# Kernel optimization log

Measured on AMD Instinct MI355X. Metric: run time of the kernel, lower is better.

Reference implementation:

```python
import jax, jax.numpy as jnp
import numpy as np

S = 32.0
M = 0.35
T = 0.2
EPS = 1e-12  # F.normalize default eps


def _l2_normalize(x, axis):
    n = jnp.sqrt(jnp.sum(x * x, axis=axis, keepdims=True))
    return x / jnp.maximum(n, EPS)


def setup_inputs() -> dict:
    key = jax.random.key(0)
    k1, k2, k3 = jax.random.split(key, 3)
    B, D, C = 512, 512, 100000
    return {
        "input": jax.random.normal(k1, (B, D), dtype=jnp.float32),
        "weight": jax.random.normal(k2, (C, D), dtype=jnp.float32),
        "label": jax.random.randint(k3, (B,), 0, C, dtype=jnp.int64),
    }


def reference(input, weight, label):
    B = input.shape[0]
    # normalized GEMM -> cosine similarities [B, C]
    cos_theta = _l2_normalize(input, 1) @ _l2_normalize(weight, 1).T
    cos_theta = jnp.clip(cos_theta, -1.0, 1.0)
    rows = jnp.arange(B)
    gt = cos_theta[rows, label][:, None]  # [B, 1]
    # MV-AM: boost hard (mis-classified-ish) logits: cos > gt - m
    hard = cos_theta > (gt - M)
    cos_theta = jnp.where(hard, (T + 1.0) * cos_theta + T, cos_theta)
    # easy_margin=False -> final_gt = gt - m; scatter into label column
    final_gt = gt - M
    cos_theta = cos_theta.at[rows, label].set(final_gt[:, 0])
    return cos_theta * S
```

## Files before the change

kernel.cpp:

```cpp
#include <hip/hip_runtime.h>
#include <hip/hip_bf16.h>


#define S_SCALE 32.0f
#define MARGIN  0.35f
#define T_BOOST 0.2f
#define EPSN    1e-12f

constexpr int Bn = 512;
constexpr int Dn = 512;
constexpr int Cn = 100000;

constexpr int BM = 256, BN = 128, BK = 32;
constexpr int PAD = 40;

typedef __attribute__((ext_vector_type(8))) short bf16x8;
typedef __attribute__((ext_vector_type(4))) float f32x4;

static __device__ inline unsigned short f32_bf16(float f) {
    unsigned int u = __float_as_uint(f);
    u += 0x7FFFu + ((u >> 16) & 1u);
    return (unsigned short)(u >> 16);
}

__global__ __launch_bounds__(256) void prep_kernel(const float* __restrict__ in,
                                                   const float* __restrict__ w,
                                                   const int* __restrict__ label,
                                                   float* __restrict__ gt,
                                                   unsigned short* __restrict__ in_h) {
    int b = blockIdx.x;
    int t = threadIdx.x;
    const float* irow = in + (size_t)b * Dn;
    int lab = label[b];
    const float* wrow = w + (size_t)lab * Dn;
    float x0 = irow[t], x1 = irow[t + 256];
    float y0 = wrow[t], y1 = wrow[t + 256];
    float s_ii = x0 * x0 + x1 * x1;
    float s_ww = y0 * y0 + y1 * y1;
    float s_iw = x0 * y0 + x1 * y1;
    #pragma unroll
    for (int off = 32; off; off >>= 1) {
        s_ii += __shfl_xor(s_ii, off);
        s_ww += __shfl_xor(s_ww, off);
        s_iw += __shfl_xor(s_iw, off);
    }
    __shared__ float r0[4], r1[4], r2[4], bc[1];
    int wid = t >> 6;
    if ((t & 63) == 0) { r0[wid] = s_ii; r1[wid] = s_ww; r2[wid] = s_iw; }
    __syncthreads();
    if (t == 0) {
        float a = r0[0] + r0[1] + r0[2] + r0[3];
        float c = r1[0] + r1[1] + r1[2] + r1[3];
        float d = r2[0] + r2[1] + r2[2] + r2[3];
        float inv_i = 1.0f / fmaxf(sqrtf(a), EPSN);
        float g = d * inv_i / fmaxf(sqrtf(c), EPSN);
        g = fminf(fmaxf(g, -1.0f), 1.0f);
        gt[b] = g;
        bc[0] = inv_i;
    }
    __syncthreads();
    float inv_i = bc[0];
    in_h[(size_t)b * Dn + t]       = f32_bf16(x0 * inv_i);
    in_h[(size_t)b * Dn + t + 256] = f32_bf16(x1 * inv_i);
}

__global__ __launch_bounds__(256) void winv_kernel(const float* __restrict__ w,
                                                   float* __restrict__ winv) {
    int row  = blockIdx.x * 4 + (threadIdx.x >> 6);
    int lane = threadIdx.x & 63;
    const float* wr = w + (size_t)row * Dn;
    f32x4 v0 = *(const f32x4*)(wr + lane * 4);
    f32x4 v1 = *(const f32x4*)(wr + 256 + lane * 4);
    float s = 0.f;
    #pragma unroll
    for (int i = 0; i < 4; ++i) s += v0[i] * v0[i] + v1[i] * v1[i];
    #pragma unroll
    for (int off = 32; off; off >>= 1) s += __shfl_xor(s, off);
    if (lane == 0) winv[row] = 1.0f / fmaxf(sqrtf(s), EPSN);
}

__global__ __launch_bounds__(512) void gemm_kernel(const unsigned short* __restrict__ in_h,
                                                   const float* __restrict__ w,
                                                   const float* __restrict__ winv,
                                                   const float* __restrict__ gt,
                                                   const int* __restrict__ label,
                                                   float* __restrict__ out) {
    __shared__ unsigned short As[BM * PAD];
    __shared__ unsigned short Bs[BN * PAD];

    int bm = blockIdx.x;
    int bn = blockIdx.y;
    int t = threadIdx.x;
    int wid = t >> 6, lane = t & 63;
    int wm = wid >> 1, wn = wid & 1;
    int l15 = lane & 15, lk = lane >> 4;

    f32x4 acc[4][4] = {};

    int arow = t >> 2, akg = t & 3;
    int brow = t >> 2, bkg = t & 3;
    int bc_glob = bn * BN + brow;
    if (bc_glob >= Cn) bc_glob = Cn - 1;
    const float* bsrc_row = w + (size_t)bc_glob * Dn;
    float bscale = winv[bc_glob];

    for (int kt = 0; kt < Dn; kt += BK) {
        {
            bf16x8 v = *(const bf16x8*)(in_h + ((size_t)(bm * BM + arow) * Dn + kt + akg * 8));
            *(bf16x8*)&As[arow * PAD + akg * 8] = v;
            int row2 = arow + 128;
            bf16x8 v2 = *(const bf16x8*)(in_h + ((size_t)(bm * BM + row2) * Dn + kt + akg * 8));
            *(bf16x8*)&As[row2 * PAD + akg * 8] = v2;
        }
        {
            const float* src = bsrc_row + kt + bkg * 8;
            f32x4 f0 = *(const f32x4*)src;
            f32x4 f1 = *(const f32x4*)(src + 4);
            bf16x8 hv;
            #pragma unroll
            for (int i = 0; i < 4; ++i) {
                hv[i]     = (short)f32_bf16(f0[i] * bscale);
                hv[4 + i] = (short)f32_bf16(f1[i] * bscale);
            }
            *(bf16x8*)&Bs[brow * PAD + bkg * 8] = hv;
        }
        __syncthreads();
        bf16x8 a[4], bb[4];
        #pragma unroll
        for (int mf = 0; mf < 4; ++mf)
            a[mf] = *(const bf16x8*)&As[(wm * 64 + mf * 16 + l15) * PAD + lk * 8];
        #pragma unroll
        for (int nf = 0; nf < 4; ++nf)
            bb[nf] = *(const bf16x8*)&Bs[(wn * 64 + nf * 16 + l15) * PAD + lk * 8];
        #pragma unroll
        for (int mf = 0; mf < 4; ++mf)
            #pragma unroll
            for (int nf = 0; nf < 4; ++nf)
                acc[mf][nf] = __builtin_amdgcn_mfma_f32_16x16x32_bf16(a[mf], bb[nf], acc[mf][nf], 0, 0, 0);
        __syncthreads();
    }

    #pragma unroll
    for (int mf = 0; mf < 4; ++mf) {
        int brow_base = bm * BM + wm * 64 + mf * 16 + lk * 4;
        #pragma unroll
        for (int r = 0; r < 4; ++r) {
            int b_row = brow_base + r;
            float g   = gt[b_row];
            int lab   = label[b_row];
            float thr = g - MARGIN;
            float gv  = thr * S_SCALE;
            size_t obase = (size_t)b_row * Cn;
            #pragma unroll
            for (int nf = 0; nf < 4; ++nf) {
                int c = bn * BN + wn * 64 + nf * 16 + l15;
                if (c < Cn) {
                    float cosv = acc[mf][nf][r];
                    cosv = fminf(fmaxf(cosv, -1.0f), 1.0f);
                    float o;
                    if (c == lab)          o = gv;
                    else if (cosv > thr)   o = ((T_BOOST + 1.0f) * cosv + T_BOOST) * S_SCALE;
                    else                   o = cosv * S_SCALE;
                    out[obase + c] = o;
                }
            }
        }
    }
}

extern "C" void kernel_launch(void* const* d_in, const int* in_sizes, int n_in,
                              void* d_out, int out_size, void* d_ws, size_t ws_size,
                              hipStream_t stream) {
    const float* in  = (const float*)d_in[0];
    const float* w   = (const float*)d_in[1];
    const int* label = (const int*)d_in[2];
    float* out = (float*)d_out;

    char* ws = (char*)d_ws;
    float* gt   = (float*)ws;
    float* winv = (float*)(ws + 4096);
    unsigned short* in_h = (unsigned short*)(ws + 4096 + 400384);

    prep_kernel<<<dim3(Bn), dim3(256), 0, stream>>>(in, w, label, gt, in_h);
    winv_kernel<<<dim3(Cn / 4), dim3(256), 0, stream>>>(w, winv);
    dim3 grid(2, (Cn + BN - 1) / BN);
    gemm_kernel<<<grid, dim3(512), 0, stream>>>(in_h, w, winv, gt, label, out);
}
```

Measured before the change: 187.1 us.

## Fuse weight-norm into GEMM with full-K swizzled LDS tile, drop winv kernel

Removes the separate winv kernel. Each GEMM block now loads its 64 weight rows for the full K=512 once, computes their norms in-register, and stores normalized bf16 into an XOR-swizzled LDS tile. The block covers all 512 batch rows, so weights are read once instead of twice, and the K loop has no per-step syncs. A operands are read directly from global (L2-resident in_h) rather than staged in LDS. This trades a large 64KB LDS tile and more accumulator registers for fewer global weight passes and one fewer launch.

```diff
diff --git a/kernel.cpp b/kernel.cpp
--- a/kernel.cpp
+++ b/kernel.cpp
@@ -10,9 +10,7 @@
 constexpr int Bn = 512;
 constexpr int Dn = 512;
 constexpr int Cn = 100000;
-
-constexpr int BM = 256, BN = 128, BK = 32;
-constexpr int PAD = 40;
+constexpr int BN = 64;
 
 typedef __attribute__((ext_vector_type(8))) short bf16x8;
 typedef __attribute__((ext_vector_type(4))) float f32x4;
@@ -64,103 +62,96 @@
     in_h[(size_t)b * Dn + t + 256] = f32_bf16(x1 * inv_i);
 }
 
-__global__ __launch_bounds__(256) void winv_kernel(const float* __restrict__ w,
-                                                   float* __restrict__ winv) {
-    int row  = blockIdx.x * 4 + (threadIdx.x >> 6);
-    int lane = threadIdx.x & 63;
-    const float* wr = w + (size_t)row * Dn;
-    f32x4 v0 = *(const f32x4*)(wr + lane * 4);
-    f32x4 v1 = *(const f32x4*)(wr + 256 + lane * 4);
-    float s = 0.f;
-    #pragma unroll
-    for (int i = 0; i < 4; ++i) s += v0[i] * v0[i] + v1[i] * v1[i];
-    #pragma unroll
-    for (int off = 32; off; off >>= 1) s += __shfl_xor(s, off);
-    if (lane == 0) winv[row] = 1.0f / fmaxf(sqrtf(s), EPSN);
-}
+__global__ __launch_bounds__(512, 4) void gemm_kernel(const unsigned short* __restrict__ in_h,
+                                                      const float* __restrict__ w,
+                                                      const float* __restrict__ gt,
+                                                      const int* __restrict__ label,
+                                                      float* __restrict__ out) {
+    __shared__ unsigned short Bs[BN * 512];
+    char* bsb = (char*)Bs;
+    int t = threadIdx.x, wid = t >> 6, lane = t & 63;
+    int cbase = blockIdx.x * BN;
 
-__global__ __launch_bounds__(512) void gemm_kernel(const unsigned short* __restrict__ in_h,
-                                                   const float* __restrict__ w,
-                                                   const float* __restrict__ winv,
-                                                   const float* __restrict__ gt,
-                                                   const int* __restrict__ label,
-                                                   float* __restrict__ out) {
-    __shared__ unsigned short As[BM * PAD];
-    __shared__ unsigned short Bs[BN * PAD];
+    {
+        int rl = (wid << 3) | (lane >> 3);
+        int rg = cbase + rl; if (rg >= Cn) rg = Cn - 1;
+        const float* wr = w + (size_t)rg * Dn;
+        int kc = lane & 7;
+        f32x4 vd[16];
+        #pragma unroll
+        for (int i = 0; i < 8; ++i) {
+            vd[2*i]   = *(const f32x4*)(wr + kc * 8 + i * 64);
+            vd[2*i+1] = *(const f32x4*)(wr + kc * 8 + i * 64 + 4);
+        }
+        float s = 0.f;
+        #pragma unroll
+        for (int j = 0; j < 16; ++j)
+            s += vd[j][0]*vd[j][0] + vd[j][1]*vd[j][1] + vd[j][2]*vd[j][2] + vd[j][3]*vd[j][3];
+        s += __shfl_xor(s, 1); s += __shfl_xor(s, 2); s += __shfl_xor(s, 4);
+        float invn = 1.0f / fmaxf(sqrtf(s), EPSN);
+        #pragma unroll
+        for (int i = 0; i < 8; ++i) {
+            bf16x8 hv;
+            #pragma unroll
+            for (int j = 0; j < 4; ++j) {
+                hv[j]     = (short)f32_bf16(vd[2*i][j]   * invn);
+                hv[4 + j] = (short)f32_bf16(vd[2*i+1][j] * invn);
+            }
+            int off = ((rl << 10) + (kc << 4) + (i << 7)) ^ ((rl & 7) << 4);
+            *(bf16x8*)(bsb + off) = hv;
+        }
+    }
+    __syncthreads();
 
-    int bm = blockIdx.x;
-    int bn = blockIdx.y;
-    int t = threadIdx.x;
-    int wid = t >> 6, lane = t & 63;
     int wm = wid >> 1, wn = wid & 1;
     int l15 = lane & 15, lk = lane >> 4;
+    const unsigned short* abase = in_h + (size_t)(wm * 128 + l15) * Dn + lk * 8;
+    int brow0 = wn * 32 + l15;
 
-    f32x4 acc[4][4] = {};
+    f32x4 acc[8][2];
+    #pragma unroll
+    for (int m = 0; m < 8; ++m)
+        #pragma unroll
+        for (int n = 0; n < 2; ++n) acc[m][n] = (f32x4){0.f, 0.f, 0.f, 0.f};
 
-    int arow = t >> 2, akg = t & 3;
-    int brow = t >> 2, bkg = t & 3;
-    int bc_glob = bn * BN + brow;
-    if (bc_glob >= Cn) bc_glob = Cn - 1;
-    const float* bsrc_row = w + (size_t)bc_glob * Dn;
-    float bscale = winv[bc_glob];
-
-    for (int kt = 0; kt < Dn; kt += BK) {
-        {
-            bf16x8 v = *(const bf16x8*)(in_h + ((size_t)(bm * BM + arow) * Dn + kt + akg * 8));
-            *(bf16x8*)&As[arow * PAD + akg * 8] = v;
-            int row2 = arow + 128;
-            bf16x8 v2 = *(const bf16x8*)(in_h + ((size_t)(bm * BM + row2) * Dn + kt + akg * 8));
-            *(bf16x8*)&As[row2 * PAD + akg * 8] = v2;
+    #pragma unroll
+    for (int kt = 0; kt < Dn; kt += 32) {
+        bf16x8 a[8], b[2];
+        #pragma unroll
+        for (int mf = 0; mf < 8; ++mf)
+            a[mf] = *(const bf16x8*)(abase + mf * 16 * Dn + kt);
+        #pragma unroll
+        for (int nf = 0; nf < 2; ++nf) {
+            int br = brow0 + nf * 16;
+            int off = ((br << 10) + kt * 2 + (lk << 4)) ^ ((br & 7) << 4);
+            b[nf] = *(const bf16x8*)(bsb + off);
         }
-        {
-            const float* src = bsrc_row + kt + bkg * 8;
-            f32x4 f0 = *(const f32x4*)src;
-            f32x4 f1 = *(const f32x4*)(src + 4);
-            bf16x8 hv;
+        #pragma unroll
+        for (int mf = 0; mf < 8; ++mf)
             #pragma unroll
-            for (int i = 0; i < 4; ++i) {
-                hv[i]     = (short)f32_bf16(f0[i] * bscale);
-                hv[4 + i] = (short)f32_bf16(f1[i] * bscale);
-            }
-            *(bf16x8*)&Bs[brow * PAD + bkg * 8] = hv;
-        }
-        __syncthreads();
-        bf16x8 a[4], bb[4];
-        #pragma unroll
-        for (int mf = 0; mf < 4; ++mf)
-            a[mf] = *(const bf16x8*)&As[(wm * 64 + mf * 16 + l15) * PAD + lk * 8];
-        #pragma unroll
-        for (int nf = 0; nf < 4; ++nf)
-            bb[nf] = *(const bf16x8*)&Bs[(wn * 64 + nf * 16 + l15) * PAD + lk * 8];
-        #pragma unroll
-        for (int mf = 0; mf < 4; ++mf)
-            #pragma unroll
-            for (int nf = 0; nf < 4; ++nf)
-                acc[mf][nf] = __builtin_amdgcn_mfma_f32_16x16x32_bf16(a[mf], bb[nf], acc[mf][nf], 0, 0, 0);
-        __syncthreads();
+            for (int nf = 0; nf < 2; ++nf)
+                acc[mf][nf] = __builtin_amdgcn_mfma_f32_16x16x32_bf16(a[mf], b[nf], acc[mf][nf], 0, 0, 0);
     }
 
     #pragma unroll
-    for (int mf = 0; mf < 4; ++mf) {
-        int brow_base = bm * BM + wm * 64 + mf * 16 + lk * 4;
+    for (int mf = 0; mf < 8; ++mf) {
         #pragma unroll
         for (int r = 0; r < 4; ++r) {
-            int b_row = brow_base + r;
+            int b_row = wm * 128 + mf * 16 + lk * 4 + r;
             float g   = gt[b_row];
             int lab   = label[b_row];
             float thr = g - MARGIN;
             float gv  = thr * S_SCALE;
             size_t obase = (size_t)b_row * Cn;
             #pragma unroll
-            for (int nf = 0; nf < 4; ++nf) {
-                int c = bn * BN + wn * 64 + nf * 16 + l15;
+            for (int nf = 0; nf < 2; ++nf) {
+                int c = cbase + wn * 32 + nf * 16 + l15;
                 if (c < Cn) {
                     float cosv = acc[mf][nf][r];
                     cosv = fminf(fmaxf(cosv, -1.0f), 1.0f);
-                    float o;
-                    if (c == lab)          o = gv;
-                    else if (cosv > thr)   o = ((T_BOOST + 1.0f) * cosv + T_BOOST) * S_SCALE;
-                    else                   o = cosv * S_SCALE;
+                    float o = (cosv > thr) ? ((T_BOOST + 1.0f) * cosv + T_BOOST) : cosv;
+                    o *= S_SCALE;
+                    if (c == lab) o = gv;
                     out[obase + c] = o;
                 }
             }
@@ -177,12 +168,9 @@
     float* out = (float*)d_out;
 
     char* ws = (char*)d_ws;
-    float* gt   = (float*)ws;
-    float* winv = (float*)(ws + 4096);
-    unsigned short* in_h = (unsigned short*)(ws + 4096 + 400384);
+    float* gt            = (float*)ws;
+    unsigned short* in_h = (unsigned short*)(ws + 4096);
 
     prep_kernel<<<dim3(Bn), dim3(256), 0, stream>>>(in, w, label, gt, in_h);
-    winv_kernel<<<dim3(Cn / 4), dim3(256), 0, stream>>>(w, winv);
-    dim3 grid(2, (Cn + BN - 1) / BN);
-    gemm_kernel<<<grid, dim3(512), 0, stream>>>(in_h, w, winv, gt, label, out);
+    gemm_kernel<<<dim3((Cn + BN - 1) / BN), dim3(512), 0, stream>>>(in_h, w, gt, label, out);
 }
```

After: 301.7 us. +61.2%, slower.
